# Optimization experiments

Hardware: AMD Instinct MI355X
Metric: run time of the kernel (lower is better)

Reference implementation:

```python
import jax, jax.numpy as jnp
import numpy as np

B, T, N = 128, 1024, 64


def setup_inputs() -> dict:
    key = jax.random.key(0)
    k1, k2, k3, k4, k5 = jax.random.split(key, 5)
    potentials = jax.random.normal(k1, (B, T, N), dtype=jnp.float32)
    tags = jax.random.randint(k2, (B, T), 0, N, dtype=jnp.int32)
    # valid lengths in [T//2, T] so every sequence has at least one step
    sequence_length = jax.random.randint(k3, (B,), T // 2, T + 1, dtype=jnp.int32)
    chain_kernel = jax.random.normal(k4, (N, N), dtype=jnp.float32)
    sample_weight = jax.random.uniform(k5, (B,), dtype=jnp.float32)
    return {
        "potentials": potentials,
        "tags": tags,
        "sequence_length": sequence_length,
        "chain_kernel": chain_kernel,
        "sample_weight": sample_weight,
    }


def _crf_sequence_score(potentials, tags, sequence_length, chain_kernel):
    # potentials: [B,T,N], tags: [B,T] int, chain_kernel: [N,N]
    Bx, Tx, Nx = potentials.shape
    t_idx = jnp.arange(Tx)
    mask = (t_idx[None, :] < sequence_length[:, None]).astype(potentials.dtype)  # [B,T]
    # unary score: potentials at the gold tag per step
    unary = jnp.take_along_axis(potentials, tags[..., None].astype(jnp.int32), axis=2)[..., 0]  # [B,T]
    unary_score = jnp.sum(unary * mask, axis=1)  # [B]
    # binary score: transitions tag[t] -> tag[t+1], valid if t+1 < seq_len
    trans_sc = chain_kernel[tags[:, :-1], tags[:, 1:]]  # [B,T-1]
    binary_score = jnp.sum(trans_sc * mask[:, 1:], axis=1)  # [B]
    return unary_score + binary_score


def _crf_log_norm(potentials, sequence_length, chain_kernel):
    # forward algorithm with lax.scan over time
    Bx, Tx, Nx = potentials.shape
    alpha0 = potentials[:, 0]  # [B,N]
    pots_rest = jnp.transpose(potentials[:, 1:], (1, 0, 2))  # [T-1,B,N]
    step_mask = (jnp.arange(1, Tx)[:, None] < sequence_length[None, :])  # [T-1,B]

    def step(alpha, inp):
        pot_t, m_t = inp  # [B,N], [B]
        # logsumexp over previous tag: alpha[b,i] + trans[i,j]
        new = jax.nn.logsumexp(alpha[:, :, None] + chain_kernel[None], axis=1) + pot_t
        alpha = jnp.where(m_t[:, None], new, alpha)
        return alpha, None

    alpha_T, _ = jax.lax.scan(step, alpha0, (pots_rest, step_mask))
    return jax.nn.logsumexp(alpha_T, axis=1)  # [B]


def reference(potentials, tags, sequence_length, chain_kernel, sample_weight):
    seq_score = _crf_sequence_score(potentials, tags, sequence_length, chain_kernel)
    log_norm = _crf_log_norm(potentials, sequence_length, chain_kernel)
    log_likelihood = seq_score - log_norm  # [B]
    crf_loss = -log_likelihood * sample_weight
    return jnp.mean(crf_loss)
```

## Files before the change

### kernel.cpp

```cpp
#include <hip/hip_runtime.h>
#include <math.h>

#define BB 128
#define TT 1024
#define NN 64
#define NCH 16
#define SCH 64

typedef __attribute__((ext_vector_type(4))) float f32x4;
typedef __attribute__((ext_vector_type(4))) short bf16x4;

__device__ __forceinline__ float wave_sum64(float v) {
#pragma unroll
  for (int o = 32; o > 0; o >>= 1) v += __shfl_xor(v, o, 64);
  return v;
}

__device__ __forceinline__ unsigned pkbf(float lo, float hi) {
  unsigned a = __float_as_uint(lo) + 0x8000u;
  unsigned b = __float_as_uint(hi) + 0x8000u;
  return __builtin_amdgcn_perm(b, a, 0x07060302u);
}

__device__ __forceinline__ unsigned pkt(float lo, float hi) {
  return __builtin_amdgcn_perm(__float_as_uint(hi), __float_as_uint(lo),
                               0x07060302u);
}

__device__ __forceinline__ int fexp(float x) {
  unsigned u = __float_as_uint(x);
  int e = (int)((u >> 23) & 0xffu) - 127;
  if ((u & 0x7f800000u) == 0) e = 0;
  return e;
}

__device__ __forceinline__ void lds_barrier() {
  asm volatile("s_waitcnt lgkmcnt(0)" ::: "memory");
  __builtin_amdgcn_s_barrier();
  __builtin_amdgcn_sched_barrier(0);
}

__global__ __launch_bounds__(256, 4) void crf_phase1(
    const float* __restrict__ pot, const int* __restrict__ tags,
    const int* __restrict__ seqlen, const float* __restrict__ K,
    unsigned* __restrict__ Hg, int* __restrict__ Eexp, float* __restrict__ score,
    float* __restrict__ accf, unsigned* __restrict__ cnt) {
  __shared__ __align__(16) float ring[4][4 * 64];
  __shared__ __align__(16) unsigned sht[4][544];
  const int wv = threadIdx.x >> 6;
  const int lane = threadIdx.x & 63;
  const int tid = blockIdx.x * 4 + wv;

  if (blockIdx.x == 0 && threadIdx.x == 0) { *accf = 0.0f; *cnt = 0u; }

  if (tid < BB) {
    const int b = tid;
    const int L = seqlen[b];
    const int* tg = tags + b * TT;
    const float* pbase = pot + (size_t)b * TT * NN;
    float acc = 0.0f;
    for (int t = lane; t < TT; t += 64) {
      if (t < L) {
        int cc = tg[t];
        float u = pbase[(size_t)t * 64 + cc];
        float tr = (t >= 1) ? K[tg[t - 1] * 64 + cc] : 0.0f;
        acc += u + tr;
      }
    }
    acc = wave_sum64(acc);
    if (lane == 0) score[b] = acc;
    return;
  }

  float* const rg = ring[wv];
  unsigned* const shp = sht[wv];

  const int idx = tid - BB;
  const int c = idx >> 9;
  const int b = (idx >> 2) & (BB - 1);
  const int g = idx & 3;
  const int L = seqlen[b];
  const int q = lane >> 4, lm = lane & 15;
  const int rb = q * 4;

  const int t0 = c * SCH + 1;
  const int tend = (L < TT) ? L : TT;
  int nsteps = tend - t0;
  if (nsteps > SCH) nsteps = SCH;

  unsigned* Hc = Hg + (size_t)(b * NCH + c) * 2048 + g * 8 * 64;
  if (nsteps <= 0) {
#pragma unroll
    for (int w = 0; w < 8; w++) {
      int c0 = g * 16 + 2 * w;
      unsigned v = (lane == c0 ? 0x3F80u : 0u) | (lane == c0 + 1 ? 0x3F800000u : 0u);
      Hc[w * 64 + lane] = v;
    }
    if (lane == 0) Eexp[(b * NCH + c) * 4 + g] = 0;
    return;
  }

  bf16x4 Af[4][4];
#pragma unroll
  for (int mt = 0; mt < 4; mt++)
#pragma unroll
    for (int kt = 0; kt < 4; kt++) {
      float v0 = __expf(K[(kt * 16 + rb + 0) * 64 + mt * 16 + lm]);
      float v1 = __expf(K[(kt * 16 + rb + 1) * 64 + mt * 16 + lm]);
      float v2 = __expf(K[(kt * 16 + rb + 2) * 64 + mt * 16 + lm]);
      float v3 = __expf(K[(kt * 16 + rb + 3) * 64 + mt * 16 + lm]);
      uint2 u; u.x = pkbf(v0, v1); u.y = pkbf(v2, v3);
      Af[mt][kt] = *(bf16x4*)&u;
    }

  f32x4 D[4];
#pragma unroll
  for (int mt = 0; mt < 4; mt++) {
    f32x4 d;
#pragma unroll
    for (int r = 0; r < 4; r++)
      d[r] = __expf(K[(g * 16 + lm) * 64 + mt * 16 + rb + r]);
    D[mt] = d;
  }

  const float* Pj = pot + (size_t)b * TT * NN + lane;
#pragma unroll
  for (int k = 0; k < 3; k++) {
    int tt = t0 + k; tt = tt > TT - 1 ? TT - 1 : tt;
    rg[k * 64 + lane] = __expf(Pj[(size_t)tt * NN]);
  }
  int t3 = t0 + 3 > TT - 1 ? TT - 1 : t0 + 3;
  int t4 = t0 + 4 > TT - 1 ? TT - 1 : t0 + 4;
  float rawq0 = Pj[(size_t)t3 * NN];
  float rawq1 = Pj[(size_t)t4 * NN];

  int etot = 0;
  int s = 0;

  f32x4 pxA[4], pxB[4];
#pragma unroll
  for (int kt = 0; kt < 4; kt++)
    pxA[kt] = *(const f32x4*)&rg[0 * 64 + kt * 16 + rb];

  while (s + 9 <= nsteps && t0 + s + 12 <= TT - 1) {
    const float* Ps = Pj + (size_t)(t0 + s) * NN;
#define STEP_F(k, PXC, PXN)                                                    \
    {                                                                          \
      if ((k) == 7) {                      \
        float d00 = __int_as_float(                                            \
            __builtin_amdgcn_readfirstlane(__float_as_int(D[0][0])));          \
        int e = fexp(d00);                                                     \
        float psc = ldexpf(1.0f, -e);                                          \
        etot += e;                                                             \
        _Pragma("unroll")                                                      \
        for (int kt = 0; kt < 4; kt++) PXC[kt] *= psc;                         \
      }                                                                        \
      bf16x4 Bf[4];                                                            \
      _Pragma("unroll")                                                        \
      for (int kt = 0; kt < 4; kt++) {                                         \
        f32x4 pr = D[kt] * PXC[kt];                                            \
        uint2 u;                                                               \
        u.x = pkt(pr[0], pr[1]);                                               \
        u.y = pkt(pr[2], pr[3]);                                               \
        Bf[kt] = *(bf16x4*)&u;                                                 \
      }                                                                        \
      _Pragma("unroll")                                                        \
      for (int kt = 0; kt < 4; kt++)                                           \
        PXN[kt] = *(const f32x4*)&rg[(((k) + 1) & 3) * 64 + kt * 16 + rb];     \
      rg[(((k) + 3) & 3) * 64 + lane] = __expf(rawq0);                         \
      rawq0 = rawq1;                                                           \
      rawq1 = Ps[(size_t)((k) + 5) * NN];                                      \
      _Pragma("unroll")                                                        \
      for (int mt = 0; mt < 4; mt++) {                                         \
        f32x4 acc = {0.f, 0.f, 0.f, 0.f};                                      \
        _Pragma("unroll")                                                      \
        for (int kt = 0; kt < 4; kt++)                                         \
          acc = __builtin_amdgcn_mfma_f32_16x16x16bf16_1k(Af[mt][kt], Bf[kt],  \
                                                          acc, 0, 0, 0);       \
        D[mt] = acc;                                                           \
      }                                                                        \
    }
    STEP_F(0, pxA, pxB)  STEP_F(1, pxB, pxA)
    STEP_F(2, pxA, pxB)  STEP_F(3, pxB, pxA)
    STEP_F(4, pxA, pxB)  STEP_F(5, pxB, pxA)
    STEP_F(6, pxA, pxB)  STEP_F(7, pxB, pxA)
#undef STEP_F
    s += 8;
  }

  f32x4 pxc[4], pxn[4];
#pragma unroll
  for (int kt = 0; kt < 4; kt++) pxc[kt] = pxA[kt];

  for (; s < nsteps - 1; s++) {
    if ((s & 7) == 7) {
      float d00 = __int_as_float(__builtin_amdgcn_readfirstlane(__float_as_int(D[0][0])));
      int e = fexp(d00);
      float psc = ldexpf(1.0f, -e);
      etot += e;
#pragma unroll
      for (int kt = 0; kt < 4; kt++) pxc[kt] *= psc;
    }
    bf16x4 Bf[4];
#pragma unroll
    for (int kt = 0; kt < 4; kt++) {
      f32x4 pr = D[kt] * pxc[kt];
      uint2 u;
      u.x = pkt(pr[0], pr[1]);
      u.y = pkt(pr[2], pr[3]);
      Bf[kt] = *(bf16x4*)&u;
    }
#pragma unroll
    for (int kt = 0; kt < 4; kt++)
      pxn[kt] = *(const f32x4*)&rg[((s + 1) & 3) * 64 + kt * 16 + rb];
    rg[((s + 3) & 3) * 64 + lane] = __expf(rawq0);
    rawq0 = rawq1;
    {
      int tn = t0 + s + 5; tn = tn > TT - 1 ? TT - 1 : tn;
      rawq1 = Pj[(size_t)tn * NN];
    }
#pragma unroll
    for (int mt = 0; mt < 4; mt++) {
      f32x4 acc = {0.f, 0.f, 0.f, 0.f};
#pragma unroll
      for (int kt = 0; kt < 4; kt++)
        acc = __builtin_amdgcn_mfma_f32_16x16x16bf16_1k(Af[mt][kt], Bf[kt], acc, 0, 0, 0);
      D[mt] = acc;
    }
#pragma unroll
    for (int kt = 0; kt < 4; kt++) pxc[kt] = pxn[kt];
  }

  {
    float hf = __int_as_float(
        __builtin_amdgcn_readfirstlane(__float_as_int(D[0][0] * pxc[0][0])));
    int ef = fexp(hf);
    float sc = ldexpf(1.0f, -ef);
    etot += ef;
#pragma unroll
    for (int mt = 0; mt < 4; mt++) {
      f32x4 d = D[mt]; f32x4 pv = pxc[mt];
      int base = lm * 33 + mt * 8 + q * 2;
      shp[base]     = pkbf(d[0] * pv[0] * sc, d[1] * pv[1] * sc);
      shp[base + 1] = pkbf(d[2] * pv[2] * sc, d[3] * pv[3] * sc);
    }
#pragma unroll
    for (int w = 0; w < 8; w++) {
      unsigned short a0 = ((const unsigned short*)(shp + (2 * w) * 33 + (lane >> 1)))[lane & 1];
      unsigned short a1 = ((const unsigned short*)(shp + (2 * w + 1) * 33 + (lane >> 1)))[lane & 1];
      Hc[w * 64 + lane] = (unsigned)a0 | ((unsigned)a1 << 16);
    }
    if (lane == 0) Eexp[(b * NCH + c) * 4 + g] = etot;
  }
}

__global__ __launch_bounds__(256, 4) void crf_phase2(
    const float* __restrict__ pot, const unsigned* __restrict__ Hg,
    const int* __restrict__ Eexp, const float* __restrict__ score,
    const float* __restrict__ wgt, float* __restrict__ accf,
    unsigned* __restrict__ cnt, float* __restrict__ out) {
  __shared__ __align__(16) float sp[2][4 * 64];
  const int g = threadIdx.x >> 6;
  const int j = threadIdx.x & 63;
  const int b = blockIdx.x;

  float a = __expf(pot[(size_t)b * TT * NN + j]);
  int atot = 0;
  const int ee = Eexp[b * 64 + j];

  const unsigned* Hb = Hg + (size_t)b * NCH * 2048 + g * 8 * 64;
  unsigned u0[8], u1[8];
#pragma unroll
  for (int w = 0; w < 8; w++) u0[w] = Hb[w * 64 + j];
#pragma unroll
  for (int w = 0; w < 8; w++) u1[w] = Hb[2048 + w * 64 + j];

#define CHUNK(cur, c)                                                          \
  do {                                                                         \
    float S = 0.0f;                                                            \
    _Pragma("unroll")                                                          \
    for (int w = 0; w < 8; w++) {                                              \
      float a0 = __shfl(a, 16 * g + 2 * w, 64);                                \
      float a1 = __shfl(a, 16 * g + 2 * w + 1, 64);                            \
      unsigned r = cur[w];                                                     \
      S += __uint_as_float(r << 16) * a0 +                                     \
           __uint_as_float(r & 0xffff0000u) * a1;                              \
    }                                                                          \
    sp[(c) & 1][g * 64 + j] = S;                                               \
    if ((c) + 2 < NCH) {   \
      const unsigned* Hn = Hb + (size_t)((c) + 2) * 2048;                      \
      _Pragma("unroll")                                                        \
      for (int w = 0; w < 8; w++) cur[w] = Hn[w * 64 + j];                     \
    }                                                                          \
    lds_barrier();                                                             \
    int e0 = __shfl(ee, (c) * 4 + 0, 64);                                      \
    int e1 = __shfl(ee, (c) * 4 + 1, 64);                                      \
    int e2 = __shfl(ee, (c) * 4 + 2, 64);                                      \
    int e3 = __shfl(ee, (c) * 4 + 3, 64);                                      \
    int em = max(max(e0, e1), max(e2, e3));                                    \
    float Sc = ldexpf(sp[(c) & 1][0 * 64 + j], e0 - em) +                      \
               ldexpf(sp[(c) & 1][1 * 64 + j], e1 - em) +                      \
               ldexpf(sp[(c) & 1][2 * 64 + j], e2 - em) +                      \
               ldexpf(sp[(c) & 1][3 * 64 + j], e3 - em);                       \
    int er = fexp(__int_as_float(                                              \
        __builtin_amdgcn_readfirstlane(__float_as_int(Sc))));                  \
    a = ldexpf(Sc, -er);                                                       \
    atot += em + er;                                                           \
  } while (0)

  CHUNK(u0, 0);  CHUNK(u1, 1);  CHUNK(u0, 2);  CHUNK(u1, 3);
  CHUNK(u0, 4);  CHUNK(u1, 5);  CHUNK(u0, 6);  CHUNK(u1, 7);
  CHUNK(u0, 8);  CHUNK(u1, 9);  CHUNK(u0, 10); CHUNK(u1, 11);
  CHUNK(u0, 12); CHUNK(u1, 13); CHUNK(u0, 14); CHUNK(u1, 15);
#undef CHUNK

  float ssum = wave_sum64(a);
  if (threadIdx.x == 0) {
    float lognorm = __logf(ssum) + (float)atot * 0.69314718055994530942f;
    float loss = -(score[b] - lognorm) * wgt[b];
    atomicAdd(accf, loss * (1.0f / BB));
    __threadfence();
    unsigned old = atomicAdd(cnt, 1u);
    if (old == BB - 1) out[0] = atomicAdd(accf, 0.0f);
  }
}

__global__ __launch_bounds__(64) void crf_main_fb(
    const float* __restrict__ pot, const int* __restrict__ tags,
    const int* __restrict__ seqlen, const float* __restrict__ K,
    float* __restrict__ ws) {
  __shared__ float sh[4096];
  const int lane = threadIdx.x;
  const int blk = blockIdx.x;
  if (blk < BB) {
    const int b = blk;
    const int L = seqlen[b];
    float Ec[64];
#pragma unroll
    for (int i = 0; i < 64; i++) Ec[i] = __expf(K[i * 64 + lane]);
    const float* pb = pot + (size_t)b * TT * NN + lane;
    float av = __expf(pb[0]);
    int etot = 0;
    sh[lane] = av;
    float pf[8];
#pragma unroll
    for (int k = 0; k < 8; k++) pf[k] = pb[(size_t)(1 + k) * 64];
    for (int t0 = 1; t0 < L; t0 += 8) {
#pragma unroll
      for (int k = 0; k < 8; k++) {
        const int t = t0 + k;
        const float pe = __expf(pf[k]);
        int tn = t + 8; tn = tn > (TT - 1) ? (TT - 1) : tn;
        pf[k] = pb[(size_t)tn * 64];
        const float4* arow = (const float4*)(sh + ((t - 1) & 1) * 64);
        float s[8];
#pragma unroll
        for (int qq = 0; qq < 8; qq++) s[qq] = 0.0f;
#pragma unroll
        for (int qq = 0; qq < 16; qq++) {
          float4 a4 = arow[qq];
          float pr = fmaf(a4.x, Ec[4 * qq + 0], fmaf(a4.y, Ec[4 * qq + 1],
                     fmaf(a4.z, Ec[4 * qq + 2], a4.w * Ec[4 * qq + 3])));
          s[qq & 7] += pr;
        }
        float S = ((s[0] + s[1]) + (s[2] + s[3])) + ((s[4] + s[5]) + (s[6] + s[7]));
        if (t < L) {
          av = S * pe;
          if ((t & 3) == 0) {
            float m0 = __shfl(av, 0, 64);
            int e = ((__float_as_int(m0) >> 23) & 0xff) - 126;
            av = ldexpf(av, -e);
            etot += e;
          }
        }
        sh[(t & 1) * 64 + lane] = av;
      }
    }
    float ssum = wave_sum64(av);
    if (lane == 0) ws[b] = __logf(ssum) + (float)etot * 0.69314718055994530942f;
  } else {
    const int b = blk - BB;
    const int L = seqlen[b];
    for (int i = lane; i < 4096; i += 64) sh[i] = K[i];
    __syncthreads();
    const int* tg = tags + b * TT;
    const float* pbase = pot + (size_t)b * TT * NN;
    float acc = 0.0f;
    for (int t = lane; t < TT; t += 64) {
      if (t < L) {
        int cc = tg[t];
        float u = pbase[(size_t)t * 64 + cc];
        float tr = 0.0f;
        if (t >= 1) tr = sh[tg[t - 1] * 64 + cc];
        acc += u + tr;
      }
    }
    acc = wave_sum64(acc);
    if (lane == 0) ws[BB + b] = acc;
  }
}

__global__ __launch_bounds__(128) void crf_combine_fb(
    const float* __restrict__ ws, const float* __restrict__ wgt,
    float* __restrict__ out) {
  const int i = threadIdx.x;
  float lv = -(ws[BB + i] - ws[i]) * wgt[i];
  lv = wave_sum64(lv);
  __shared__ float p[2];
  if ((i & 63) == 0) p[i >> 6] = lv;
  __syncthreads();
  if (i == 0) out[0] = (p[0] + p[1]) * (1.0f / 128.0f);
}

extern "C" void kernel_launch(void* const* d_in, const int* in_sizes, int n_in,
                              void* d_out, int out_size, void* d_ws, size_t ws_size,
                              hipStream_t stream) {
  const float* pot    = (const float*)d_in[0];
  const int*   tags   = (const int*)d_in[1];
  const int*   seqlen = (const int*)d_in[2];
  const float* K      = (const float*)d_in[3];
  const float* wgt    = (const float*)d_in[4];

  const size_t HG_DW = (size_t)BB * NCH * 2048;
  const size_t NEXP  = (size_t)BB * NCH * 4;
  const size_t need  = (HG_DW + NEXP + BB + 2) * 4;

  if (ws_size >= need) {
    unsigned* Hg    = (unsigned*)d_ws;
    int* Eexp       = (int*)(Hg + HG_DW);
    float* score    = (float*)(Eexp + NEXP);
    float* accf     = score + BB;
    unsigned* cntp  = (unsigned*)(accf + 1);
    crf_phase1<<<(BB + BB * NCH * 4) / 4, 256, 0, stream>>>(pot, tags, seqlen, K,
                                                            Hg, Eexp, score, accf,
                                                            cntp);
    crf_phase2<<<BB, 256, 0, stream>>>(pot, Hg, Eexp, score, wgt, accf, cntp,
                                       (float*)d_out);
  } else {
    float* ws = (float*)d_ws;
    crf_main_fb<<<256, 64, 0, stream>>>(pot, tags, seqlen, K, ws);
    crf_combine_fb<<<1, 128, 0, stream>>>(ws, wgt, (float*)d_out);
  }
}
```

Measured before the change: 161.9 us.

## Process two column groups per wave in CRF phase1 chunk propagation

Each phase1 wave now propagates two 16-column groups of the chunk transfer matrix instead of one, sharing the exp(K) A-fragments, the potential ring buffer and the prefetch loads across both. This halves the number of chunk waves launched and interleaves two independent MFMA chains to hide MFMA latency. In exchange it doubles per-wave register and LDS use, which may lower occupancy. Group B is rescaled using group A's exponent, which could affect numerical range.

Result: slower. 169.1 us (+4.4%).

```diff
diff --git a/kernel.cpp b/kernel.cpp
--- a/kernel.cpp
+++ b/kernel.cpp
@@ -46,7 +46,7 @@
     unsigned* __restrict__ Hg, int* __restrict__ Eexp, float* __restrict__ score,
     float* __restrict__ accf, unsigned* __restrict__ cnt) {
   __shared__ __align__(16) float ring[4][4 * 64];
-  __shared__ __align__(16) unsigned sht[4][544];
+  __shared__ __align__(16) unsigned sht[4][1088];
   const int wv = threadIdx.x >> 6;
   const int lane = threadIdx.x & 63;
   const int tid = blockIdx.x * 4 + wv;
@@ -73,12 +73,14 @@
   }
 
   float* const rg = ring[wv];
-  unsigned* const shp = sht[wv];
+  unsigned* const shpA = sht[wv];
+  unsigned* const shpB = sht[wv] + 544;
 
   const int idx = tid - BB;
-  const int c = idx >> 9;
-  const int b = (idx >> 2) & (BB - 1);
-  const int g = idx & 3;
+  const int c = idx >> 8;
+  const int b = (idx >> 1) & (BB - 1);
+  const int g0 = idx & 1;
+  const int gA = 2 * g0, gB = 2 * g0 + 1;
   const int L = seqlen[b];
   const int q = lane >> 4, lm = lane & 15;
   const int rb = q * 4;
@@ -88,15 +90,22 @@
   int nsteps = tend - t0;
   if (nsteps > SCH) nsteps = SCH;
 
-  unsigned* Hc = Hg + (size_t)(b * NCH + c) * 2048 + g * 8 * 64;
+  unsigned* HcA = Hg + (size_t)(b * NCH + c) * 2048 + gA * 8 * 64;
+  unsigned* HcB = Hg + (size_t)(b * NCH + c) * 2048 + gB * 8 * 64;
   if (nsteps <= 0) {
 #pragma unroll
     for (int w = 0; w < 8; w++) {
-      int c0 = g * 16 + 2 * w;
-      unsigned v = (lane == c0 ? 0x3F80u : 0u) | (lane == c0 + 1 ? 0x3F800000u : 0u);
-      Hc[w * 64 + lane] = v;
-    }
-    if (lane == 0) Eexp[(b * NCH + c) * 4 + g] = 0;
+      int cA = gA * 16 + 2 * w;
+      unsigned vA = (lane == cA ? 0x3F80u : 0u) | (lane == cA + 1 ? 0x3F800000u : 0u);
+      HcA[w * 64 + lane] = vA;
+      int cB = gB * 16 + 2 * w;
+      unsigned vB = (lane == cB ? 0x3F80u : 0u) | (lane == cB + 1 ? 0x3F800000u : 0u);
+      HcB[w * 64 + lane] = vB;
+    }
+    if (lane == 0) {
+      Eexp[(b * NCH + c) * 4 + gA] = 0;
+      Eexp[(b * NCH + c) * 4 + gB] = 0;
+    }
     return;
   }
 
@@ -113,14 +122,16 @@
       Af[mt][kt] = *(bf16x4*)&u;
     }
 
-  f32x4 D[4];
+  f32x4 DA[4], DB[4];
 #pragma unroll
   for (int mt = 0; mt < 4; mt++) {
-    f32x4 d;
-#pragma unroll
-    for (int r = 0; r < 4; r++)
-      d[r] = __expf(K[(g * 16 + lm) * 64 + mt * 16 + rb + r]);
-    D[mt] = d;
+    f32x4 dA, dB;
+#pragma unroll
+    for (int r = 0; r < 4; r++) {
+      dA[r] = __expf(K[(gA * 16 + lm) * 64 + mt * 16 + rb + r]);
+      dB[r] = __expf(K[(gB * 16 + lm) * 64 + mt * 16 + rb + r]);
+    }
+    DA[mt] = dA; DB[mt] = dB;
   }
 
   const float* Pj = pot + (size_t)b * TT * NN + lane;
@@ -134,7 +145,7 @@
   float rawq0 = Pj[(size_t)t3 * NN];
   float rawq1 = Pj[(size_t)t4 * NN];
 
-  int etot = 0;
+  int etotA = 0, etotB = 0;
   int s = 0;
 
   f32x4 pxA[4], pxB[4];
@@ -146,23 +157,28 @@
     const float* Ps = Pj + (size_t)(t0 + s) * NN;
 #define STEP_F(k, PXC, PXN)                                                    \
     {                                                                          \
-      if ((k) == 7) {                      \
-        float d00 = __int_as_float(                                            \
-            __builtin_amdgcn_readfirstlane(__float_as_int(D[0][0])));          \
-        int e = fexp(d00);                                                     \
-        float psc = ldexpf(1.0f, -e);                                          \
-        etot += e;                                                             \
+      if ((k) == 7) {            \
+        float dA0 = __int_as_float(                                            \
+            __builtin_amdgcn_readfirstlane(__float_as_int(DA[0][0])));         \
+        float dB0 = __int_as_float(                                            \
+            __builtin_amdgcn_readfirstlane(__float_as_int(DB[0][0])));         \
+        int eA = fexp(dA0), eB = fexp(dB0);                                    \
+        float pscA = ldexpf(1.0f, -eA);                                        \
+        float corrB = ldexpf(1.0f, eA - eB);                                   \
+        etotA += eA; etotB += eB;                                              \
         _Pragma("unroll")                                                      \
-        for (int kt = 0; kt < 4; kt++) PXC[kt] *= psc;                         \
+        for (int kt = 0; kt < 4; kt++) { PXC[kt] *= pscA; DB[kt] *= corrB; }   \
       }                                                                        \
-      bf16x4 Bf[4];                                                            \
+      bf16x4 BfA[4], BfB[4];                                                   \
       _Pragma("unroll")                                                        \
       for (int kt = 0; kt < 4; kt++) {                                         \
-        f32x4 pr = D[kt] * PXC[kt];                                            \
-        uint2 u;                                                               \
-        u.x = pkt(pr[0], pr[1]);                                               \
-        u.y = pkt(pr[2], pr[3]);                                               \
-        Bf[kt] = *(bf16x4*)&u;                                                 \
+        f32x4 prA = DA[kt] * PXC[kt];                                          \
+        f32x4 prB = DB[kt] * PXC[kt];                                          \
+        uint2 uA, uB;                                                          \
+        uA.x = pkt(prA[0], prA[1]); uA.y = pkt(prA[2], prA[3]);                \
+        uB.x = pkt(prB[0], prB[1]); uB.y = pkt(prB[2], prB[3]);                \
+        BfA[kt] = *(bf16x4*)&uA;                                               \
+        BfB[kt] = *(bf16x4*)&uB;                                               \
       }                                                                        \
       _Pragma("unroll")                                                        \
       for (int kt = 0; kt < 4; kt++)                                           \
@@ -172,12 +188,16 @@
       rawq1 = Ps[(size_t)((k) + 5) * NN];                                      \
       _Pragma("unroll")                                                        \
       for (int mt = 0; mt < 4; mt++) {                                         \
-        f32x4 acc = {0.f, 0.f, 0.f, 0.f};                                      \
+        f32x4 aA = {0.f, 0.f, 0.f, 0.f};                                       \
+        f32x4 aB = {0.f, 0.f, 0.f, 0.f};                                       \
         _Pragma("unroll")                                                      \
-        for (int kt = 0; kt < 4; kt++)                                         \
-          acc = __builtin_amdgcn_mfma_f32_16x16x16bf16_1k(Af[mt][kt], Bf[kt],  \
-                                                          acc, 0, 0, 0);       \
-        D[mt] = acc;                                                           \
+        for (int kt = 0; kt < 4; kt++) {                                       \
+          aA = __builtin_amdgcn_mfma_f32_16x16x16bf16_1k(Af[mt][kt], BfA[kt],  \
+                                                         aA, 0, 0, 0);         \
+          aB = __builtin_amdgcn_mfma_f32_16x16x16bf16_1k(Af[mt][kt], BfB[kt],  \
+                                                         aB, 0, 0, 0);         \
+        }                                                                      \
+        DA[mt] = aA; DB[mt] = aB;                                              \
       }                                                                        \
     }
     STEP_F(0, pxA, pxB)  STEP_F(1, pxB, pxA)
@@ -194,21 +214,25 @@
 
   for (; s < nsteps - 1; s++) {
     if ((s & 7) == 7) {
-      float d00 = __int_as_float(__builtin_amdgcn_readfirstlane(__float_as_int(D[0][0])));
-      int e = fexp(d00);
-      float psc = ldexpf(1.0f, -e);
-      etot += e;
-#pragma unroll
-      for (int kt = 0; kt < 4; kt++) pxc[kt] *= psc;
-    }
-    bf16x4 Bf[4];
+      float dA0 = __int_as_float(__builtin_amdgcn_readfirstlane(__float_as_int(DA[0][0])));
+      float dB0 = __int_as_float(__builtin_amdgcn_readfirstlane(__float_as_int(DB[0][0])));
+      int eA = fexp(dA0), eB = fexp(dB0);
+      float pscA = ldexpf(1.0f, -eA);
+      float corrB = ldexpf(1.0f, eA - eB);
+      etotA += eA; etotB += eB;
+#pragma unroll
+      for (int kt = 0; kt < 4; kt++) { pxc[kt] *= pscA; DB[kt] *= corrB; }
+    }
+    bf16x4 BfA[4], BfB[4];
 #pragma unroll
     for (int kt = 0; kt < 4; kt++) {
-      f32x4 pr = D[kt] * pxc[kt];
-      uint2 u;
-      u.x = pkt(pr[0], pr[1]);
-      u.y = pkt(pr[2], pr[3]);
-      Bf[kt] = *(bf16x4*)&u;
+      f32x4 prA = DA[kt] * pxc[kt];
+      f32x4 prB = DB[kt] * pxc[kt];
+      uint2 uA, uB;
+      uA.x = pkt(prA[0], prA[1]); uA.y = pkt(prA[2], prA[3]);
+      uB.x = pkt(prB[0], prB[1]); uB.y = pkt(prB[2], prB[3]);
+      BfA[kt] = *(bf16x4*)&uA;
+      BfB[kt] = *(bf16x4*)&uB;
     }
 #pragma unroll
     for (int kt = 0; kt < 4; kt++)
@@ -221,36 +245,52 @@
     }
 #pragma unroll
     for (int mt = 0; mt < 4; mt++) {
-      f32x4 acc = {0.f, 0.f, 0.f, 0.f};
-#pragma unroll
-      for (int kt = 0; kt < 4; kt++)
-        acc = __builtin_amdgcn_mfma_f32_16x16x16bf16_1k(Af[mt][kt], Bf[kt], acc, 0, 0, 0);
-      D[mt] = acc;
+      f32x4 aA = {0.f, 0.f, 0.f, 0.f};
+      f32x4 aB = {0.f, 0.f, 0.f, 0.f};
+#pragma unroll
+      for (int kt = 0; kt < 4; kt++) {
+        aA = __builtin_amdgcn_mfma_f32_16x16x16bf16_1k(Af[mt][kt], BfA[kt], aA, 0, 0, 0);
+        aB = __builtin_amdgcn_mfma_f32_16x16x16bf16_1k(Af[mt][kt], BfB[kt], aB, 0, 0, 0);
+      }
+      DA[mt] = aA; DB[mt] = aB;
     }
 #pragma unroll
     for (int kt = 0; kt < 4; kt++) pxc[kt] = pxn[kt];
   }
 
   {
-    float hf = __int_as_float(
-        __builtin_amdgcn_readfirstlane(__float_as_int(D[0][0] * pxc[0][0])));
-    int ef = fexp(hf);
-    float sc = ldexpf(1.0f, -ef);
-    etot += ef;
+    float hfA = __int_as_float(
+        __builtin_amdgcn_readfirstlane(__float_as_int(DA[0][0] * pxc[0][0])));
+    float hfB = __int_as_float(
+        __builtin_amdgcn_readfirstlane(__float_as_int(DB[0][0] * pxc[0][0])));
+    int efA = fexp(hfA), efB = fexp(hfB);
+    float scA = ldexpf(1.0f, -efA);
+    float scB = ldexpf(1.0f, -efB);
+    etotA += efA; etotB += efB;
 #pragma unroll
     for (int mt = 0; mt < 4; mt++) {
-      f32x4 d = D[mt]; f32x4 pv = pxc[mt];
+      f32x4 d = DA[mt]; f32x4 pv = pxc[mt];
       int base = lm * 33 + mt * 8 + q * 2;
-      shp[base]     = pkbf(d[0] * pv[0] * sc, d[1] * pv[1] * sc);
-      shp[base + 1] = pkbf(d[2] * pv[2] * sc, d[3] * pv[3] * sc);
-    }
+      shpA[base]     = pkbf(d[0] * pv[0] * scA, d[1] * pv[1] * scA);
+      shpA[base + 1] = pkbf(d[2] * pv[2] * scA, d[3] * pv[3] * scA);
+      f32x4 e = DB[mt];
+      shpB[base]     = pkbf(e[0] * pv[0] * scB, e[1] * pv[1] * scB);
+      shpB[base + 1] = pkbf(e[2] * pv[2] * scB, e[3] * pv[3] * scB);
+    }
+    asm volatile("" ::: "memory");
 #pragma unroll
     for (int w = 0; w < 8; w++) {
-      unsigned short a0 = ((const unsigned short*)(shp + (2 * w) * 33 + (lane >> 1)))[lane & 1];
-      unsigned short a1 = ((const unsigned short*)(shp + (2 * w + 1) * 33 + (lane >> 1)))[lane & 1];
-      Hc[w * 64 + lane] = (unsigned)a0 | ((unsigned)a1 << 16);
-    }
-    if (lane == 0) Eexp[(b * NCH + c) * 4 + g] = etot;
+      unsigned short a0 = ((const unsigned short*)(shpA + (2 * w) * 33 + (lane >> 1)))[lane & 1];
+      unsigned short a1 = ((const unsigned short*)(shpA + (2 * w + 1) * 33 + (lane >> 1)))[lane & 1];
+      HcA[w * 64 + lane] = (unsigned)a0 | ((unsigned)a1 << 16);
+      unsigned short b0 = ((const unsigned short*)(shpB + (2 * w) * 33 + (lane >> 1)))[lane & 1];
+      unsigned short b1 = ((const unsigned short*)(shpB + (2 * w + 1) * 33 + (lane >> 1)))[lane & 1];
+      HcB[w * 64 + lane] = (unsigned)b0 | ((unsigned)b1 << 16);
+    }
+    if (lane == 0) {
+      Eexp[(b * NCH + c) * 4 + gA] = etotA;
+      Eexp[(b * NCH + c) * 4 + gB] = etotB;
+    }
   }
 }
 
@@ -431,7 +471,7 @@
     float* score    = (float*)(Eexp + NEXP);
     float* accf     = score + BB;
     unsigned* cntp  = (unsigned*)(accf + 1);
-    crf_phase1<<<(BB + BB * NCH * 4) / 4, 256, 0, stream>>>(pot, tags, seqlen, K,
+    crf_phase1<<<(BB + BB * NCH * 2) / 4, 256, 0, stream>>>(pot, tags, seqlen, K,
                                                             Hg, Eexp, score, accf,
                                                             cntp);
     crf_phase2<<<BB, 256, 0, stream>>>(pot, Hg, Eexp, score, wgt, accf, cntp,
```
